# Kernel optimization log

Measured on AMD Instinct MI355X. Metric: run time of the kernel, lower is better.

The kernel has to match this reference:

```python
import jax, jax.numpy as jnp
import numpy as np
from jax import lax

KSIZE = 3
STRIDE = 1
RATE = 2
SCALE = 10.0
GROUPS = 4
RATES = (1, 2, 4, 8)
ESCAPE_NAN = 1e-4


def extract_patches(x, kernel, stride):
    # x: [N,C,H,W]; ZeroPad2d(1) when kernel != 1, then sliding windows.
    pad = 0 if kernel == 1 else 1
    x = jnp.pad(x, ((0, 0), (0, 0), (pad, pad), (pad, pad)))
    N, C, H, W = x.shape
    oh = (H - kernel) // stride + 1
    ow = (W - kernel) // stride + 1
    r = jnp.arange(oh)[:, None] * stride + jnp.arange(kernel)[None, :]  # [oh,k]
    c = jnp.arange(ow)[:, None] * stride + jnp.arange(kernel)[None, :]  # [ow,k]
    p = x[:, :, r[:, :, None, None], c[None, None, :, :]]  # [N,C,oh,k,ow,k]
    p = p.transpose(0, 2, 4, 1, 3, 5)  # [N,oh,ow,C,k,k] (matches torch unfold order)
    return p.reshape(N, oh * ow, C, kernel, kernel)


def make_mask_c(H, W):
    # Vectorized version of the O(H*W) nested python loop: 4-neighbor patch bias.
    ii, jj = jnp.meshgrid(jnp.arange(H), jnp.arange(W), indexing='ij')
    p = ii * W + jj
    mc = jnp.zeros((H * W, H, W), jnp.float32)
    mc = mc.at[p[:, 1:] - 1, ii[:, 1:], jj[:, 1:]].set(1.0)        # j>=1
    mc = mc.at[p[:, :-1] + 1, ii[:, :-1], jj[:, :-1]].set(1.0)     # j<=W-2
    mc = mc.at[p[:-1] + W, ii[:-1], jj[:-1]].set(1.0)              # i<=H-2
    mc = mc.at[p[1:] - W, ii[1:], jj[1:]].set(1.0)                 # i>=1
    return mc


def atn_conv(x1, x2, mask, mask_all, fuse_w, fuse_b):
    N, C1, H1, W1 = x1.shape
    _, C2, H2, W2 = x2.shape
    kernel = 2 * RATE
    # patch banks
    raw_w = extract_patches(x1, kernel, RATE * STRIDE)          # [N,L,C1,4,4]
    w = extract_patches(x2, KSIZE, STRIDE)                      # [N,L,C2,3,3]
    # mask interpolated to x2 size with align_corners=True == identity here
    m = extract_patches(mask, KSIZE, STRIDE)                    # [N,L,1,3,3]
    m = m.mean(axis=(2, 3, 4))                                  # [N,L]
    mm = (m == 0.0).astype(x2.dtype)                            # 1 = valid patch
    mask_c = make_mask_c(H2, W2)                                # [L,H2,W2]
    pad = 0 if KSIZE == 1 else 1
    kt = kernel - 1 - 1  # conv_transpose padding=1 -> equiv fwd pad k-1-p

    def per_batch(xi, wi, raw_wi, mi, ma):
        # xi [C2,H2,W2], wi [L,C2,3,3], raw_wi [L,C1,4,4], mi [L], ma [1,H2,W2]
        norm = jnp.sqrt(jnp.sum(wi * wi, axis=(1, 2, 3), keepdims=True))
        wi_n = wi / jnp.maximum(norm, ESCAPE_NAN)
        yi = lax.conv_general_dilated(xi[None], wi_n, (1, 1), [(pad, pad), (pad, pad)],
                                      dimension_numbers=('NCHW', 'OIHW', 'NCHW'))[0]  # [L,H2,W2]
        mi_b = mi[:, None, None]
        yi = yi * mi_b * ma
        yi = jax.nn.softmax(yi * SCALE, axis=0)
        yi = yi + yi * mask_c * 0.5
        yi = yi * mi_b * ma
        yi = jnp.maximum(yi, 1e-8)
        # conv_transpose2d(yi, raw_wi, stride=RATE, padding=1)
        w_t = jnp.flip(raw_wi, axis=(-2, -1))  # [L,C1,4,4] used as IOHW
        out = lax.conv_general_dilated(yi[None], w_t, (1, 1), [(kt, kt), (kt, kt)],
                                       lhs_dilation=(RATE, RATE),
                                       dimension_numbers=('NCHW', 'IOHW', 'NCHW'))[0]
        return out / 4.0  # [C1,H1,W1]

    y = jax.vmap(per_batch)(x2, w, raw_w, mm, mask_all)          # [N,C1,H1,W1]

    # fuse: 4 dilated conv+relu branches, concat on channels
    outs = []
    for g in range(GROUPS):
        d = RATES[g]
        o = lax.conv_general_dilated(y, fuse_w[g], (1, 1), [(d, d), (d, d)],
                                     rhs_dilation=(d, d),
                                     dimension_numbers=('NCHW', 'OIHW', 'NCHW'))
        outs.append(jax.nn.relu(o + fuse_b[g][None, :, None, None]))
    return jnp.concatenate(outs, axis=1)


def setup_inputs() -> dict:
    key = jax.random.key(0)
    k1, k2, k3, k4, k5 = jax.random.split(key, 5)
    N, C, H2, W2 = 2, 128, 48, 48
    x1 = jax.random.normal(k1, (N, C, 2 * H2, 2 * W2), jnp.float32)
    x2 = jax.random.normal(k2, (N, C, H2, W2), jnp.float32)
    mask = jnp.zeros((N, 1, H2, W2), jnp.float32).at[:, :, 12:36, 12:36].set(1.0)  # 1 = hole
    mask_all = jax.random.uniform(k3, (N, 1, H2, W2), jnp.float32)
    out_pg = 64 // GROUPS
    fuse_w = jax.random.normal(k4, (GROUPS, out_pg, C, 3, 3), jnp.float32) * 0.02
    fuse_b = jax.random.normal(k5, (GROUPS, out_pg), jnp.float32) * 0.02
    return {'x1': x1, 'x2': x2, 'mask': mask, 'mask_all': mask_all,
            'fuse_w': fuse_w, 'fuse_b': fuse_b}


def reference(x1, x2, mask, mask_all, fuse_w, fuse_b):
    return atn_conv(x1, x2, mask, mask_all, fuse_w, fuse_b)
```

## Files before the change

### kernel.cpp

```cpp
#include <hip/hip_runtime.h>
#include <math.h>

typedef unsigned short u16;
typedef unsigned int   u32;
typedef float f32x4 __attribute__((ext_vector_type(4)));
typedef short bfx8  __attribute__((ext_vector_type(8)));

#define NB   2
#define CCH  128
#define HS   48
#define LL   2304
#define KW   2048
#define HO   96
#define PIX  9216
#define VHALF ((size_t)LL * KW)

#define XTH_B 0
#define XTL_B 1179648
#define PXN_B 2359296
#define NRM_B 2377728
#define MM_B  2396160
#define WF_B  2414592
#define WT_B  2562048
#define S_B   11999232
#define TBD_B S_B
#define V_B   (S_B + 10616832)
#define Z_B   33232896
#define YT_B  54466560
#define CMAP_B 59185152
#define LIDX_B (CMAP_B + 18432)
#define MET_B  (LIDX_B + 18432)

__device__ __forceinline__ u16 f2bf(float f) {
    u32 u = __float_as_uint(f);
    u32 r = (u + 0x7fffu + ((u >> 16) & 1u)) >> 16;
    return (u16)r;
}
__device__ __forceinline__ float bf2f(u16 h) {
    return __uint_as_float(((u32)h) << 16);
}
__device__ __forceinline__ void gll16(const void* g, void* l) {
    __builtin_amdgcn_global_load_lds((const __attribute__((address_space(1))) void*)g,
                                     (__attribute__((address_space(3))) void*)l, 16, 0, 0);
}

__global__ __launch_bounds__(256) void xprep_k(const float* __restrict__ x2,
                                               u16* __restrict__ Xh, u16* __restrict__ Xl,
                                               float* __restrict__ pxn) {
    __shared__ float lt[32][130];
    int n = blockIdx.z;
    int pix0 = blockIdx.x * 32;
    int tid = threadIdx.x;
    #pragma unroll
    for (int i = tid; i < 32 * 128; i += 256) {
        int c = i >> 5, p = i & 31;
        lt[p][c] = x2[((size_t)(n * CCH + c)) * LL + pix0 + p];
    }
    __syncthreads();
    #pragma unroll
    for (int i = tid; i < 32 * 128; i += 256) {
        int p = i >> 7, c = i & 127;
        float v = lt[p][c];
        u16 h = f2bf(v);
        size_t o = (size_t)(n * LL + pix0 + p) * CCH + c;
        Xh[o] = h;
        Xl[o] = f2bf(v - bf2f(h));
    }
    if (tid < 32) {
        float s = 0.0f;
        for (int c = 0; c < CCH; c++) { float t = lt[tid][c]; s += t * t; }
        pxn[n * LL + pix0 + tid] = s;
    }
}

__global__ __launch_bounds__(256) void boxnorm_k(const float* __restrict__ pxn,
                                                 const float* __restrict__ mask,
                                                 float* __restrict__ rnorm,
                                                 float* __restrict__ mmb) {
    int n = blockIdx.z;
    int p = blockIdx.x * 256 + threadIdx.x;
    int i = p / HS, j = p - (p / HS) * HS;
    float s = 0.0f, msum = 0.0f;
    for (int di = -1; di <= 1; di++)
        for (int dj = -1; dj <= 1; dj++) {
            int ii = i + di, jj = j + dj;
            if (ii >= 0 && ii < HS && jj >= 0 && jj < HS) {
                s += pxn[n * LL + ii * HS + jj];
                msum += mask[(n * HS + ii) * HS + jj];
            }
        }
    rnorm[n * LL + p] = 1.0f / fmaxf(sqrtf(s), 1e-4f);
    mmb[n * LL + p] = (msum == 0.0f) ? 1.0f : 0.0f;
}

__global__ __launch_bounds__(256) void scan_k(const float* __restrict__ mmb,
                                              int* __restrict__ cmap,
                                              int* __restrict__ lidx,
                                              int* __restrict__ meta) {
    int n = blockIdx.x;
    int tid = threadIdx.x, lane = tid & 63, wid = tid >> 6;
    __shared__ int wtot[4];
    int base = tid * 9;
    int flags[9], cnt = 0;
    #pragma unroll
    for (int e = 0; e < 9; e++) {
        flags[e] = (mmb[n * LL + base + e] != 0.0f) ? 1 : 0;
        cnt += flags[e];
    }
    int inc = cnt;
    #pragma unroll
    for (int o = 1; o < 64; o <<= 1) {
        int v = __shfl_up(inc, o);
        if (lane >= o) inc += v;
    }
    if (lane == 63) wtot[wid] = inc;
    __syncthreads();
    int woff = 0;
    for (int wv = 0; wv < wid; wv++) woff += wtot[wv];
    int k = woff + inc - cnt;
    #pragma unroll
    for (int e = 0; e < 9; e++) {
        int l = base + e;
        if (flags[e]) { cmap[n * LL + l] = k; lidx[n * LL + k] = l; k++; }
        else cmap[n * LL + l] = -1;
    }
    if (tid == 255) {
        int Knz = woff + inc;
        int KA = ((Knz + 191) / 192) * 64;
        if (KA < 64) KA = 64;
        meta[n * 2] = Knz;
        meta[n * 2 + 1] = KA;
    }
}

__global__ __launch_bounds__(256) void sgemm_k(const u16* __restrict__ Xh, const u16* __restrict__ Xl,
                                               float* __restrict__ S) {
    __shared__ __align__(16) u16 Ah[4096], Al[4096], Bh[4096], Bl[4096];
    int tid = threadIdx.x, w = tid >> 6, lane = tid & 63;
    int t = blockIdx.x, bi = 0;
    while (t >= 18 - bi) { t -= 18 - bi; bi++; }
    int bj = bi + t;
    int m0 = bi * 128, n0 = bj * 128;
    int srow = lane & 15, sk = (lane >> 4) * 8;
    size_t a1 = (size_t)(m0 + w * 16 + srow) * CCH + sk;
    size_t a2 = a1 + (size_t)64 * CCH;
    size_t b1 = (size_t)(n0 + w * 16 + srow) * CCH + sk;
    size_t b2 = b1 + (size_t)64 * CCH;
    int wm = (w >> 1) * 64, wn = (w & 1) * 64;
    int ga = (w >> 1) * 4, gb = (w & 1) * 4;
    f32x4 acc[4][4];
    #pragma unroll
    for (int i = 0; i < 4; i++)
        #pragma unroll
        for (int j = 0; j < 4; j++) acc[i][j] = (f32x4)0.0f;

    for (int k0 = 0; k0 < CCH; k0 += 32) {
        if (k0) __syncthreads();
        gll16(Xh + a1 + k0, Ah + w * 512);
        gll16(Xh + a2 + k0, Ah + (w + 4) * 512);
        gll16(Xl + a1 + k0, Al + w * 512);
        gll16(Xl + a2 + k0, Al + (w + 4) * 512);
        gll16(Xh + b1 + k0, Bh + w * 512);
        gll16(Xh + b2 + k0, Bh + (w + 4) * 512);
        gll16(Xl + b1 + k0, Bl + w * 512);
        gll16(Xl + b2 + k0, Bl + (w + 4) * 512);
        __syncthreads();
        bfx8 ah[4], al[4], bh[4], bl[4];
        #pragma unroll
        for (int i = 0; i < 4; i++) {
            ah[i] = *(const bfx8*)&Ah[(ga + i) * 512 + lane * 8];
            al[i] = *(const bfx8*)&Al[(ga + i) * 512 + lane * 8];
        }
        #pragma unroll
        for (int j = 0; j < 4; j++) {
            bh[j] = *(const bfx8*)&Bh[(gb + j) * 512 + lane * 8];
            bl[j] = *(const bfx8*)&Bl[(gb + j) * 512 + lane * 8];
        }
        #pragma unroll
        for (int i = 0; i < 4; i++)
            #pragma unroll
            for (int j = 0; j < 4; j++) {
                acc[i][j] = __builtin_amdgcn_mfma_f32_16x16x32_bf16(ah[i], bh[j], acc[i][j], 0, 0, 0);
                acc[i][j] = __builtin_amdgcn_mfma_f32_16x16x32_bf16(ah[i], bl[j], acc[i][j], 0, 0, 0);
                acc[i][j] = __builtin_amdgcn_mfma_f32_16x16x32_bf16(al[i], bh[j], acc[i][j], 0, 0, 0);
            }
    }
    #pragma unroll
    for (int j = 0; j < 4; j++) {
        int col = n0 + wn + j * 16 + (lane & 15);
        #pragma unroll
        for (int i = 0; i < 4; i++) {
            int rbase = m0 + wm + i * 16 + (lane >> 4) * 4;
            #pragma unroll
            for (int r = 0; r < 4; r++)
                S[(size_t)(rbase + r) * LL + col] = acc[i][j][r];
            if (bi != bj)
                *(f32x4*)&S[(size_t)col * LL + rbase] = acc[i][j];
        }
    }
}

__global__ __launch_bounds__(256) void zsum_k(const float* __restrict__ S,
                                              float* __restrict__ Z) {
    __shared__ float lt[3][48][49];
    int t = blockIdx.x, pi = 0;
    while (t >= HS - pi) { t -= HS - pi; pi++; }
    int li = pi + t;
    int tid = threadIdx.x;
    #pragma unroll
    for (int di = 0; di < 3; di++) {
        int a = pi + di - 1, b = li + di - 1;
        bool valid = (a >= 0) && (a < HS) && (b >= 0) && (b < HS);
        const float* base = S + ((size_t)a * HS) * LL + b * HS;
        #pragma unroll
        for (int k = 0; k < 9; k++) {
            int idx = tid + k * 256;
            int r = idx / HS, c = idx - r * HS;
            lt[di][r][c] = valid ? base[(size_t)r * LL + c] : 0.0f;
        }
    }
    __syncthreads();
    #pragma unroll
    for (int k = 0; k < 9; k++) {
        int idx = tid + k * 256;
        int pj = idx / HS, lj = idx - pj * HS;
        float acc = 0.0f;
        #pragma unroll
        for (int dj = -1; dj <= 1; dj++) {
            int rr = pj + dj, cc = lj + dj;
            if (rr >= 0 && rr < HS && cc >= 0 && cc < HS)
                acc += lt[0][rr][cc] + lt[1][rr][cc] + lt[2][rr][cc];
        }
        Z[((size_t)pi * HS + pj) * LL + li * HS + lj] = acc;
    }
    if (pi != li) {
        #pragma unroll
        for (int k = 0; k < 9; k++) {
            int idx = tid + k * 256;
            int lj = idx / HS, pj = idx - lj * HS;
            float acc = 0.0f;
            #pragma unroll
            for (int dj = -1; dj <= 1; dj++) {
                int rr = pj + dj, cc = lj + dj;
                if (rr >= 0 && rr < HS && cc >= 0 && cc < HS)
                    acc += lt[0][rr][cc] + lt[1][rr][cc] + lt[2][rr][cc];
            }
            Z[((size_t)li * HS + lj) * LL + pi * HS + pj] = acc;
        }
    }
}

__global__ __launch_bounds__(256) void softmax_k(const float* __restrict__ Z,
                                                 u16* __restrict__ Tbc,
                                                 const float* __restrict__ rnorm,
                                                 const float* __restrict__ mmb,
                                                 const float* __restrict__ mask_all,
                                                 const int* __restrict__ cmap,
                                                 const int* __restrict__ meta, int n) {
    int p = blockIdx.x, tid = threadIdx.x;
    __shared__ float red[8];
    const float* row = Z + (size_t)p * LL;
    u16* orow = Tbc + (size_t)p * LL;
    float ma = mask_all[n * LL + p];
    float v[9], m9[9];
    float mx = -3.0e38f;
    #pragma unroll
    for (int e = 0; e < 9; e++) {
        int l = tid + e * 256;
        float m_ = mmb[n * LL + l];
        m9[e] = m_;
        float s = row[l] * rnorm[n * LL + l] * m_ * ma * 10.0f;
        v[e] = s;
        mx = fmaxf(mx, s);
    }
    #pragma unroll
    for (int o = 32; o; o >>= 1) mx = fmaxf(mx, __shfl_down(mx, o));
    int wid = tid >> 6, lane = tid & 63;
    if (lane == 0) red[wid] = mx;
    __syncthreads();
    mx = fmaxf(fmaxf(red[0], red[1]), fmaxf(red[2], red[3]));
    float sum = 0.0f;
    #pragma unroll
    for (int e = 0; e < 9; e++) { v[e] = __expf(v[e] - mx); sum += v[e]; }
    #pragma unroll
    for (int o = 32; o; o >>= 1) sum += __shfl_down(sum, o);
    if (lane == 0) red[4 + wid] = sum;
    __syncthreads();
    float inv = 1.0f / (red[4] + red[5] + red[6] + red[7]);
    int pi = p / HS, pj = p - (p / HS) * HS;
    #pragma unroll
    for (int e = 0; e < 9; e++) {
        int l = tid + e * 256;
        int cm = cmap[n * LL + l];
        if (cm >= 0) {
            int li = l / HS, lj = l - li * HS;
            bool nb = (li == pi && (lj == pj - 1 || lj == pj + 1)) ||
                      (lj == pj && (li == pi - 1 || li == pi + 1));
            float z = v[e] * inv * (nb ? 1.5f : 1.0f) * m9[e] * ma;
            orow[cm] = f2bf(fmaxf(z, 1e-8f));
        }
    }
    int Knz = meta[n * 2], KA3 = 3 * meta[n * 2 + 1];
    for (int k = Knz + tid; k < KA3; k += 256) orow[k] = 0;
}

__global__ __launch_bounds__(256) void build_W_k(const float* __restrict__ x1,
                                                 u16* __restrict__ Wtc,
                                                 const int* __restrict__ lidx,
                                                 const int* __restrict__ meta, int n) {
    int idx = blockIdx.x * 256 + threadIdx.x;
    int k = idx % LL, f = idx / LL;
    int Knz = meta[n * 2];
    u16 out = 0;
    if (k < Knz) {
        int l = lidx[n * LL + k];
        int c = f & 127, tap = f >> 7;
        int ky = tap >> 2, kx = tap & 3;
        int li = l / HS, lj = l - (l / HS) * HS;
        int yy = 2 * li - 1 + ky, xx = 2 * lj - 1 + kx;
        float v = 0.0f;
        if (yy >= 0 && yy < HO && xx >= 0 && xx < HO)
            v = x1[((n * CCH + c) * HO + yy) * HO + xx];
        out = f2bf(v);
    }
    Wtc[idx] = out;
}

__global__ __launch_bounds__(256) void gemm2_k(const u16* __restrict__ Tbc, const u16* __restrict__ Wtc,
                                               u16* __restrict__ V,
                                               const int* __restrict__ meta, int n) {
    __shared__ __align__(16) u16 As[8192], Bs[8192];
    int tid = threadIdx.x, w = tid >> 6, lane = tid & 63;
    int m0 = blockIdx.x * 128, n0 = blockIdx.y * 128;
    int KA = meta[n * 2 + 1];
    int koff = blockIdx.z * KA;
    int srow = lane & 15, sk = (lane >> 4) * 8;
    size_t a1 = (size_t)(m0 + w * 16 + srow) * LL + koff + sk;
    size_t a2 = a1 + (size_t)64 * LL;
    size_t b1 = (size_t)(n0 + w * 16 + srow) * LL + koff + sk;
    size_t b2 = b1 + (size_t)64 * LL;
    int wm = (w >> 1) * 64, wn = (w & 1) * 64;
    int ga = (w >> 1) * 4, gb = (w & 1) * 4;
    f32x4 acc[4][4];
    #pragma unroll
    for (int i = 0; i < 4; i++)
        #pragma unroll
        for (int j = 0; j < 4; j++) acc[i][j] = (f32x4)0.0f;

    for (int k0 = 0; k0 < KA; k0 += 64) {
        if (k0) __syncthreads();
        gll16(Tbc + a1 + k0,      As + w * 1024);
        gll16(Tbc + a1 + k0 + 32, As + w * 1024 + 512);
        gll16(Tbc + a2 + k0,      As + (w + 4) * 1024);
        gll16(Tbc + a2 + k0 + 32, As + (w + 4) * 1024 + 512);
        gll16(Wtc + b1 + k0,      Bs + w * 1024);
        gll16(Wtc + b1 + k0 + 32, Bs + w * 1024 + 512);
        gll16(Wtc + b2 + k0,      Bs + (w + 4) * 1024);
        gll16(Wtc + b2 + k0 + 32, Bs + (w + 4) * 1024 + 512);
        __syncthreads();
        #pragma unroll
        for (int kk = 0; kk < 2; kk++) {
            bfx8 af[4], bf[4];
            #pragma unroll
            for (int i = 0; i < 4; i++) af[i] = *(const bfx8*)&As[(ga + i) * 1024 + kk * 512 + lane * 8];
            #pragma unroll
            for (int j = 0; j < 4; j++) bf[j] = *(const bfx8*)&Bs[(gb + j) * 1024 + kk * 512 + lane * 8];
            #pragma unroll
            for (int i = 0; i < 4; i++)
                #pragma unroll
                for (int j = 0; j < 4; j++)
                    acc[i][j] = __builtin_amdgcn_mfma_f32_16x16x32_bf16(af[i], bf[j], acc[i][j], 0, 0, 0);
        }
    }
    u16* Vb = V + (size_t)blockIdx.z * VHALF;
    #pragma unroll
    for (int j = 0; j < 4; j++) {
        int f = n0 + wn + j * 16 + (lane & 15);
        #pragma unroll
        for (int i = 0; i < 4; i++) {
            int rbase = m0 + wm + i * 16 + (lane >> 4) * 4;
            #pragma unroll
            for (int r = 0; r < 4; r++)
                Vb[(size_t)(rbase + r) * KW + f] = f2bf(0.25f * acc[i][j][r]);
        }
    }
}

__global__ __launch_bounds__(256) void gather_k(const u16* __restrict__ V,
                                                u16* __restrict__ yT, int n) {
    int idx = blockIdx.x * 256 + threadIdx.x;
    int c = idx & 127, pix = idx >> 7;
    int yy = pix / HO, xx = pix - yy * HO;
    int ky0 = (yy + 1) & 1, kx0 = (xx + 1) & 1;
    float s = 0.0f;
    #pragma unroll
    for (int a = 0; a < 2; a++) {
        int ky = ky0 + a * 2;
        int py = yy + 1 - ky;
        if (py < 0 || py >= HO) continue;
        int pi = py >> 1;
        #pragma unroll
        for (int b = 0; b < 2; b++) {
            int kx = kx0 + b * 2;
            int px = xx + 1 - kx;
            if (px < 0 || px >= HO) continue;
            int pj = px >> 1;
            size_t off = (size_t)(pi * HS + pj) * KW + (ky * 4 + kx) * 128 + c;
            s += bf2f(V[off]) + bf2f(V[VHALF + off]) + bf2f(V[2 * VHALF + off]);
        }
    }
    yT[(size_t)(n * PIX + pix) * CCH + c] = f2bf(s);
}

__global__ __launch_bounds__(256) void wprep_k(const float* __restrict__ fw,
                                               u16* __restrict__ Wf) {
    int idx = blockIdx.x * 256 + threadIdx.x;
    int c = idx & 127;
    int tap = (idx >> 7) % 9;
    int go = idx / (128 * 9);
    Wf[idx] = f2bf(fw[((size_t)go * 128 + c) * 9 + tap]);
}

__global__ __launch_bounds__(256) void fuse_mfma_k(const u16* __restrict__ yT,
                                                   const u16* __restrict__ Wf,
                                                   const float* __restrict__ fb,
                                                   float* __restrict__ out) {
    int n = blockIdx.z, g = blockIdx.y;
    const int d = 1 << g;
    int tid = threadIdx.x, wv = tid >> 6, lane = tid & 63;
    int pix0 = blockIdx.x * 64 + wv * 16;
    int h = pix0 / HO, w0 = pix0 - h * HO;
    int m = lane & 15, q = lane >> 4;
    int oc = m;
    const u16* brow = Wf + ((size_t)(g * 16 + oc) * 9) * CCH + q * 8;
    f32x4 acc = (f32x4)0.0f;

    #pragma unroll
    for (int tap = 0; tap < 9; tap++) {
        int dy = (tap / 3 - 1) * d, dx = (tap % 3 - 1) * d;
        int hh = h + dy;
        int ww = w0 + m + dx;
        bool v = (hh >= 0) & (hh < HO) & (ww >= 0) & (ww < HO);
        const u16* arow = yT + ((size_t)(n * PIX + hh * HO + ww)) * CCH + q * 8;
        const u16* bt = brow + tap * CCH;
        #pragma unroll
        for (int c0 = 0; c0 < CCH; c0 += 32) {
            bfx8 af = (bfx8)0;
            if (v) af = *(const bfx8*)(arow + c0);
            bfx8 bf = *(const bfx8*)(bt + c0);
            acc = __builtin_amdgcn_mfma_f32_16x16x32_bf16(af, bf, acc, 0, 0, 0);
        }
    }
    float bias = fb[g * 16 + oc];
    f32x4 o;
    #pragma unroll
    for (int r = 0; r < 4; r++) o[r] = fmaxf(acc[r] + bias, 0.0f);
    size_t oi = ((size_t)(n * 64 + g * 16 + oc)) * PIX + pix0 + q * 4;
    *(f32x4*)&out[oi] = o;
}

extern "C" void kernel_launch(void* const* d_in, const int* in_sizes, int n_in,
                              void* d_out, int out_size, void* d_ws, size_t ws_size,
                              hipStream_t stream) {
    const float* x1       = (const float*)d_in[0];
    const float* x2       = (const float*)d_in[1];
    const float* mask     = (const float*)d_in[2];
    const float* mask_all = (const float*)d_in[3];
    const float* fw       = (const float*)d_in[4];
    const float* fb       = (const float*)d_in[5];
    float* out = (float*)d_out;
    char* wsb  = (char*)d_ws;

    u16*   Xh    = (u16*)(wsb + XTH_B);
    u16*   Xl    = (u16*)(wsb + XTL_B);
    float* pxn   = (float*)(wsb + PXN_B);
    float* rnorm = (float*)(wsb + NRM_B);
    float* mmb   = (float*)(wsb + MM_B);
    u16*   Wf    = (u16*)(wsb + WF_B);
    u16*   Wtc   = (u16*)(wsb + WT_B);
    float* S     = (float*)(wsb + S_B);
    u16*   Tbc   = (u16*)(wsb + TBD_B);
    u16*   V     = (u16*)(wsb + V_B);
    float* Z     = (float*)(wsb + Z_B);
    u16*   yT    = (u16*)(wsb + YT_B);
    int*   cmap  = (int*)(wsb + CMAP_B);
    int*   lidx  = (int*)(wsb + LIDX_B);
    int*   meta  = (int*)(wsb + MET_B);

    wprep_k<<<(64 * 9 * 128) / 256, 256, 0, stream>>>(fw, Wf);
    xprep_k<<<dim3(LL / 32, 1, NB), 256, 0, stream>>>(x2, Xh, Xl, pxn);
    boxnorm_k<<<dim3(LL / 256, 1, NB), 256, 0, stream>>>(pxn, mask, rnorm, mmb);
    scan_k<<<NB, 256, 0, stream>>>(mmb, cmap, lidx, meta);

    for (int n = 0; n < NB; n++) {
        sgemm_k<<<171, 256, 0, stream>>>(Xh + (size_t)n * LL * CCH,
                                         Xl + (size_t)n * LL * CCH, S);
        zsum_k<<<HS * (HS + 1) / 2, 256, 0, stream>>>(S, Z);
        softmax_k<<<LL, 256, 0, stream>>>(Z, Tbc, rnorm, mmb, mask_all, cmap, meta, n);
        build_W_k<<<(KW * LL) / 256, 256, 0, stream>>>(x1, Wtc, lidx, meta, n);
        gemm2_k<<<dim3(18, 16, 3), 256, 0, stream>>>(Tbc, Wtc, V, meta, n);
        gather_k<<<(PIX * 128) / 256, 256, 0, stream>>>(V, yT, n);
    }
    fuse_mfma_k<<<dim3(PIX / 64, 4, NB), 256, 0, stream>>>(yT, Wf, fb, out);
}
```

Measured before the change: 325.6 us.

## Fuse box-sum with blockwise softmax statistics and write bf16 exp tiles

Merges the 3x3 box-sum kernel with a per-tile exponentiation step. Each tile computes its local row max and sum and writes bf16 exponentials instead of fp32 Z. A new fixup kernel combines the per-tile statistics online-softmax style, rescales, and compacts into Tbc. The sgemm now writes the transposed block only for the adjacent off-diagonal block that zsum reads. This is meant to halve the intermediate traffic and drop a full fp32 row read, at the cost of serial 48-element loops in one wave and bf16 rounding of the unnormalized exponentials.

```diff
diff --git a/kernel.cpp b/kernel.cpp
--- a/kernel.cpp
+++ b/kernel.cpp
@@ -23,13 +23,15 @@
 #define WF_B  2414592
 #define WT_B  2562048
 #define S_B   11999232
-#define TBD_B S_B
-#define V_B   (S_B + 10616832)
-#define Z_B   33232896
+#define TBC_B S_B
+#define V_B   22616064
+#define TBU_B 33232896
 #define YT_B  54466560
 #define CMAP_B 59185152
 #define LIDX_B (CMAP_B + 18432)
 #define MET_B  (LIDX_B + 18432)
+#define STM_B  59222048
+#define STS_B  59664416
 
 __device__ __forceinline__ u16 f2bf(float f) {
     u32 u = __float_as_uint(f);
@@ -185,6 +187,7 @@
                 acc[i][j] = __builtin_amdgcn_mfma_f32_16x16x32_bf16(al[i], bh[j], acc[i][j], 0, 0, 0);
             }
     }
+    bool wrT = (bj == bi + 1);
     #pragma unroll
     for (int j = 0; j < 4; j++) {
         int col = n0 + wn + j * 16 + (lane & 15);
@@ -194,15 +197,24 @@
             #pragma unroll
             for (int r = 0; r < 4; r++)
                 S[(size_t)(rbase + r) * LL + col] = acc[i][j][r];
-            if (bi != bj)
+            if (wrT)
                 *(f32x4*)&S[(size_t)col * LL + rbase] = acc[i][j];
         }
     }
 }
 
-__global__ __launch_bounds__(256) void zsum_k(const float* __restrict__ S,
-                                              float* __restrict__ Z) {
+__global__ __launch_bounds__(256) void zsumexp_k(const float* __restrict__ S,
+                                                 const float* __restrict__ rnorm,
+                                                 const float* __restrict__ mmb,
+                                                 const float* __restrict__ mask_all,
+                                                 u16* __restrict__ Tbu,
+                                                 float* __restrict__ statm,
+                                                 float* __restrict__ stats, int n) {
     __shared__ float lt[3][48][49];
+    __shared__ float zt[48][49];
+    __shared__ float rcA[48], mmA[48], maA[48];
+    __shared__ float rcB[48], mmB[48], maB[48];
+    __shared__ float rowm[48];
     int t = blockIdx.x, pi = 0;
     while (t >= HS - pi) { t -= HS - pi; pi++; }
     int li = pi + t;
@@ -219,6 +231,16 @@
             lt[di][r][c] = valid ? base[(size_t)r * LL + c] : 0.0f;
         }
     }
+    if (tid < 48) {
+        int lcol = n * LL + li * HS + tid;
+        rcA[tid] = rnorm[lcol] * 10.0f;
+        mmA[tid] = mmb[lcol];
+        maB[tid] = mask_all[lcol];
+        int pcol = n * LL + pi * HS + tid;
+        rcB[tid] = rnorm[pcol] * 10.0f;
+        mmB[tid] = mmb[pcol];
+        maA[tid] = mask_all[pcol];
+    }
     __syncthreads();
     #pragma unroll
     for (int k = 0; k < 9; k++) {
@@ -231,63 +253,92 @@
             if (rr >= 0 && rr < HS && cc >= 0 && cc < HS)
                 acc += lt[0][rr][cc] + lt[1][rr][cc] + lt[2][rr][cc];
         }
-        Z[((size_t)pi * HS + pj) * LL + li * HS + lj] = acc;
+        zt[pj][lj] = acc;
+    }
+    __syncthreads();
+    if (tid < 48) {
+        float ma_ = maA[tid];
+        float m = -3.0e38f;
+        for (int lj = 0; lj < 48; lj++)
+            if (mmA[lj] != 0.0f) m = fmaxf(m, zt[tid][lj] * rcA[lj] * ma_);
+        float s = 0.0f;
+        if (m > -1.0e37f)
+            for (int lj = 0; lj < 48; lj++)
+                if (mmA[lj] != 0.0f) s += __expf(zt[tid][lj] * rcA[lj] * ma_ - m);
+        rowm[tid] = m;
+        statm[(size_t)(pi * HS + tid) * HS + li] = m;
+        stats[(size_t)(pi * HS + tid) * HS + li] = s;
+    }
+    __syncthreads();
+    #pragma unroll
+    for (int k = 0; k < 9; k++) {
+        int idx = tid + k * 256;
+        int pj = idx / HS, lj = idx - pj * HS;
+        float lg = zt[pj][lj] * rcA[lj] * maA[pj];
+        Tbu[(size_t)(pi * HS + pj) * LL + li * HS + lj] = f2bf(__expf(lg - rowm[pj]));
     }
     if (pi != li) {
+        __syncthreads();
+        if (tid < 48) {
+            float ma_ = maB[tid];
+            float m = -3.0e38f;
+            for (int pj = 0; pj < 48; pj++)
+                if (mmB[pj] != 0.0f) m = fmaxf(m, zt[pj][tid] * rcB[pj] * ma_);
+            float s = 0.0f;
+            if (m > -1.0e37f)
+                for (int pj = 0; pj < 48; pj++)
+                    if (mmB[pj] != 0.0f) s += __expf(zt[pj][tid] * rcB[pj] * ma_ - m);
+            rowm[tid] = m;
+            statm[(size_t)(li * HS + tid) * HS + pi] = m;
+            stats[(size_t)(li * HS + tid) * HS + pi] = s;
+        }
+        __syncthreads();
         #pragma unroll
         for (int k = 0; k < 9; k++) {
             int idx = tid + k * 256;
             int lj = idx / HS, pj = idx - lj * HS;
-            float acc = 0.0f;
-            #pragma unroll
-            for (int dj = -1; dj <= 1; dj++) {
-                int rr = pj + dj, cc = lj + dj;
-                if (rr >= 0 && rr < HS && cc >= 0 && cc < HS)
-                    acc += lt[0][rr][cc] + lt[1][rr][cc] + lt[2][rr][cc];
-            }
-            Z[((size_t)li * HS + lj) * LL + pi * HS + pj] = acc;
-        }
-    }
-}
-
-__global__ __launch_bounds__(256) void softmax_k(const float* __restrict__ Z,
-                                                 u16* __restrict__ Tbc,
-                                                 const float* __restrict__ rnorm,
-                                                 const float* __restrict__ mmb,
-                                                 const float* __restrict__ mask_all,
-                                                 const int* __restrict__ cmap,
-                                                 const int* __restrict__ meta, int n) {
+            float lg = zt[pj][lj] * rcB[pj] * maB[lj];
+            Tbu[(size_t)(li * HS + lj) * LL + pi * HS + pj] = f2bf(__expf(lg - rowm[lj]));
+        }
+    }
+}
+
+__global__ __launch_bounds__(256) void fixup_k(const u16* __restrict__ Tbu,
+                                               u16* __restrict__ Tbc,
+                                               const float* __restrict__ statm,
+                                               const float* __restrict__ stats,
+                                               const float* __restrict__ mask_all,
+                                               const int* __restrict__ cmap,
+                                               const int* __restrict__ meta, int n) {
     int p = blockIdx.x, tid = threadIdx.x;
-    __shared__ float red[8];
-    const float* row = Z + (size_t)p * LL;
-    u16* orow = Tbc + (size_t)p * LL;
+    __shared__ float fac[48];
+    __shared__ float red[2];
+    int Knz = meta[n * 2], KA3 = 3 * meta[n * 2 + 1];
+    float nmask = (float)(LL - Knz);
+    float mb = (tid < 48) ? statm[(size_t)p * HS + tid] : -3.0e38f;
+    if (tid < 64) {
+        float m = mb;
+        #pragma unroll
+        for (int o = 32; o; o >>= 1) m = fmaxf(m, __shfl_down(m, o));
+        if (tid == 0) red[0] = (nmask > 0.0f) ? fmaxf(m, 0.0f) : m;
+    }
+    __syncthreads();
+    float m = red[0];
+    if (tid < 64) {
+        float sb = 0.0f;
+        if (tid < 48) {
+            float f = __expf(mb - m);
+            fac[tid] = f;
+            sb = stats[(size_t)p * HS + tid] * f;
+        }
+        #pragma unroll
+        for (int o = 32; o; o >>= 1) sb += __shfl_down(sb, o);
+        if (tid == 0) red[1] = 1.0f / (sb + nmask * __expf(-m));
+    }
+    __syncthreads();
+    float inv = red[1];
+    int pi = p / HS, pj = p - pi * HS;
     float ma = mask_all[n * LL + p];
-    float v[9], m9[9];
-    float mx = -3.0e38f;
-    #pragma unroll
-    for (int e = 0; e < 9; e++) {
-        int l = tid + e * 256;
-        float m_ = mmb[n * LL + l];
-        m9[e] = m_;
-        float s = row[l] * rnorm[n * LL + l] * m_ * ma * 10.0f;
-        v[e] = s;
-        mx = fmaxf(mx, s);
-    }
-    #pragma unroll
-    for (int o = 32; o; o >>= 1) mx = fmaxf(mx, __shfl_down(mx, o));
-    int wid = tid >> 6, lane = tid & 63;
-    if (lane == 0) red[wid] = mx;
-    __syncthreads();
-    mx = fmaxf(fmaxf(red[0], red[1]), fmaxf(red[2], red[3]));
-    float sum = 0.0f;
-    #pragma unroll
-    for (int e = 0; e < 9; e++) { v[e] = __expf(v[e] - mx); sum += v[e]; }
-    #pragma unroll
-    for (int o = 32; o; o >>= 1) sum += __shfl_down(sum, o);
-    if (lane == 0) red[4 + wid] = sum;
-    __syncthreads();
-    float inv = 1.0f / (red[4] + red[5] + red[6] + red[7]);
-    int pi = p / HS, pj = p - (p / HS) * HS;
     #pragma unroll
     for (int e = 0; e < 9; e++) {
         int l = tid + e * 256;
@@ -296,12 +347,11 @@
             int li = l / HS, lj = l - li * HS;
             bool nb = (li == pi && (lj == pj - 1 || lj == pj + 1)) ||
                       (lj == pj && (li == pi - 1 || li == pi + 1));
-            float z = v[e] * inv * (nb ? 1.5f : 1.0f) * m9[e] * ma;
-            orow[cm] = f2bf(fmaxf(z, 1e-8f));
-        }
-    }
-    int Knz = meta[n * 2], KA3 = 3 * meta[n * 2 + 1];
-    for (int k = Knz + tid; k < KA3; k += 256) orow[k] = 0;
+            float w = bf2f(Tbu[(size_t)p * LL + l]) * fac[li] * inv * (nb ? 1.5f : 1.0f) * ma;
+            Tbc[(size_t)p * LL + cm] = f2bf(fmaxf(w, 1e-8f));
+        }
+    }
+    for (int k = Knz + tid; k < KA3; k += 256) Tbc[(size_t)p * LL + k] = 0;
 }
 
 __global__ __launch_bounds__(256) void build_W_k(const float* __restrict__ x1,
@@ -479,13 +529,15 @@
     u16*   Wf    = (u16*)(wsb + WF_B);
     u16*   Wtc   = (u16*)(wsb + WT_B);
     float* S     = (float*)(wsb + S_B);
-    u16*   Tbc   = (u16*)(wsb + TBD_B);
+    u16*   Tbc   = (u16*)(wsb + TBC_B);
+    u16*   Tbu   = (u16*)(wsb + TBU_B);
     u16*   V     = (u16*)(wsb + V_B);
-    float* Z     = (float*)(wsb + Z_B);
     u16*   yT    = (u16*)(wsb + YT_B);
     int*   cmap  = (int*)(wsb + CMAP_B);
     int*   lidx  = (int*)(wsb + LIDX_B);
     int*   meta  = (int*)(wsb + MET_B);
+    float* statm = (float*)(wsb + STM_B);
+    float* stats = (float*)(wsb + STS_B);
 
     wprep_k<<<(64 * 9 * 128) / 256, 256, 0, stream>>>(fw, Wf);
     xprep_k<<<dim3(LL / 32, 1, NB), 256, 0, stream>>>(x2, Xh, Xl, pxn);
@@ -495,8 +547,9 @@
     for (int n = 0; n < NB; n++) {
         sgemm_k<<<171, 256, 0, stream>>>(Xh + (size_t)n * LL * CCH,
                                          Xl + (size_t)n * LL * CCH, S);
-        zsum_k<<<HS * (HS + 1) / 2, 256, 0, stream>>>(S, Z);
-        softmax_k<<<LL, 256, 0, stream>>>(Z, Tbc, rnorm, mmb, mask_all, cmap, meta, n);
+        zsumexp_k<<<HS * (HS + 1) / 2, 256, 0, stream>>>(S, rnorm, mmb, mask_all,
+                                                         Tbu, statm, stats, n);
+        fixup_k<<<LL, 256, 0, stream>>>(Tbu, Tbc, statm, stats, mask_all, cmap, meta, n);
         build_W_k<<<(KW * LL) / 256, 256, 0, stream>>>(x1, Wtc, lidx, meta, n);
         gemm2_k<<<dim3(18, 16, 3), 256, 0, stream>>>(Tbc, Wtc, V, meta, n);
         gather_k<<<(PIX * 128) / 256, 256, 0, stream>>>(V, yT, n);
```

New measurement: 390.3 us. 1.2x slower.
